# Optimization experiments

Hardware: AMD Instinct MI355X
Metric: run time of the kernel (lower is better)

## Reference

```python
import jax, jax.numpy as jnp
import numpy as np

B, T, D, H = 256, 512, 128, 256

def setup_inputs() -> dict:
    key = jax.random.key(0)
    ks = jax.random.split(key, 10)
    s_in = 1.0 / np.sqrt(H + D)
    s_td = 1.0 / np.sqrt(D)
    return {
        "x": jax.random.normal(ks[0], (B, T, D), dtype=jnp.float32),
        "delta": jax.random.uniform(ks[1], (B, T, D), dtype=jnp.float32),
        "W_mu": jax.random.uniform(ks[2], (H + D, H), minval=-s_in, maxval=s_in),
        "b_mu": jax.random.uniform(ks[3], (H,), minval=-s_in, maxval=s_in),
        "W_r": jax.random.uniform(ks[4], (H + D, H), minval=-s_in, maxval=s_in),
        "b_r": jax.random.uniform(ks[5], (H,), minval=-s_in, maxval=s_in),
        "W_h": jax.random.uniform(ks[6], (H + D, H), minval=-s_in, maxval=s_in),
        "b_h": jax.random.uniform(ks[7], (H,), minval=-s_in, maxval=s_in),
        "W_td": jax.random.uniform(ks[8], (D, H), minval=-s_td, maxval=s_td),
        "b_td": jax.random.uniform(ks[9], (H,), minval=-s_td, maxval=s_td),
    }

def reference(x, delta, W_mu, b_mu, W_r, b_r, W_h, b_h, W_td, b_td):
    # GRU-D style GRUI encoder; dropout is identity (eval mode).
    # Precompute temporal decay for all steps at once: beta [B,T,H]
    beta = jnp.exp(-jax.nn.relu(jnp.einsum('btd,dh->bth', delta, W_td) + b_td))
    # Precompute the x-part of the gate GEMMs (W split: first H rows act on h, last D on x)
    Wh_r, Wx_r = W_r[:H], W_r[H:]
    Wh_mu, Wx_mu = W_mu[:H], W_mu[H:]
    Wh_h, Wx_h = W_h[:H], W_h[H:]
    gx_r = jnp.einsum('btd,dh->bth', x, Wx_r) + b_r    # [B,T,H]
    gx_mu = jnp.einsum('btd,dh->bth', x, Wx_mu) + b_mu
    gx_h = jnp.einsum('btd,dh->bth', x, Wx_h) + b_h

    def step(h, inputs):
        beta_t, gxr_t, gxm_t, gxh_t = inputs
        h = beta_t * h
        r_t = jax.nn.sigmoid(h @ Wh_r + gxr_t)
        mu_t = jax.nn.sigmoid(h @ Wh_mu + gxm_t)
        h_hat = jnp.tanh((r_t * h) @ Wh_h + gxh_t)
        h = (1.0 - mu_t) * h + mu_t * h_hat
        return h, None

    h0 = jnp.zeros((x.shape[0], H), dtype=x.dtype)
    seq = (beta.transpose(1, 0, 2), gx_r.transpose(1, 0, 2),
           gx_mu.transpose(1, 0, 2), gx_h.transpose(1, 0, 2))
    h_T, _ = jax.lax.scan(step, h0, seq)
    return h_T
```

## Files before the change

kernel.cpp:

```cpp
#include <hip/hip_runtime.h>
#include <stdint.h>

#define TT 512
#define HB 256
#define DD 128

typedef _Float16 h2_t __attribute__((ext_vector_type(2)));
typedef _Float16 h8_t __attribute__((ext_vector_type(8)));
typedef float    f4_t __attribute__((ext_vector_type(4)));
typedef uint32_t u4_t __attribute__((ext_vector_type(4)));

#define GX_SZ 67108864ull


__device__ __forceinline__ uint32_t pack_h2f(float lo, float hi) {
  h2_t h; h[0] = (_Float16)lo; h[1] = (_Float16)hi;
  return __builtin_bit_cast(uint32_t, h);
}

__device__ __forceinline__ float fdot2f(uint32_t a, uint32_t b, float c) {
  h2_t ha = __builtin_bit_cast(h2_t, a), hb = __builtin_bit_cast(h2_t, b);
#if __has_builtin(__builtin_amdgcn_fdot2)
  return __builtin_amdgcn_fdot2(ha, hb, c, false);
#else
  return c + (float)ha[0]*(float)hb[0] + (float)ha[1]*(float)hb[1];
#endif
}

__device__ __forceinline__ void barrier_lds() {
  asm volatile("s_waitcnt lgkmcnt(0)" ::: "memory");
  __builtin_amdgcn_s_barrier();
  __builtin_amdgcn_sched_barrier(0);
}

__global__ __launch_bounds__(256)
void pack_w(const float* __restrict__ Wr, const float* __restrict__ Wmu,
            const float* __restrict__ Wh, const float* __restrict__ Wtd,
            uint8_t* __restrict__ bt) {
  const int id = blockIdx.x * 256 + threadIdx.x;
  const int a = id >> 14, rem = id & 16383;
  const int c = rem >> 6, kp = rem & 63;
  const float* W = (a==0) ? Wr : (a==1) ? Wmu : (a==2) ? Wh : Wtd;
  const int r0 = (a==3) ? 0 : 256;
  const uint32_t v = pack_h2f(W[(r0 + 2*kp)*256 + c], W[(r0 + 2*kp + 1)*256 + c]);
  *(uint32_t*)(bt + a*65536 + c*256 + ((kp*4) ^ ((c & 7) << 4))) = v;
}

__global__ __launch_bounds__(256, 2)
void gemm_pre(const float* __restrict__ x, const float* __restrict__ delta,
              const float* __restrict__ br, const float* __restrict__ bmu,
              const float* __restrict__ bh, const float* __restrict__ btd,
              const uint8_t* __restrict__ bt, uint8_t* __restrict__ ws) {
  __shared__ uint8_t BT[65536];
  const int a  = blockIdx.x & 3;
  const int m0 = (blockIdx.x >> 2) * 128;
  const int tid = threadIdx.x;
  const int l = tid & 63, w = tid >> 6;
  const float* Asrc = (a == 3) ? delta : x;
  const float* bias = (a==0) ? br : (a==1) ? bmu : (a==2) ? bh : btd;

  {
    const u4_t* s4 = (const u4_t*)(bt + (size_t)a*65536);
    u4_t* d4 = (u4_t*)BT;
    #pragma unroll
    for (int i = 0; i < 16; i++) d4[i*256 + tid] = s4[i*256 + tid];
  }
  __syncthreads();

  f4_t acc[2][16];
  #pragma unroll
  for (int rt = 0; rt < 2; rt++)
    #pragma unroll
    for (int nt = 0; nt < 16; nt++) acc[rt][nt] = (f4_t){0.f, 0.f, 0.f, 0.f};

  const int rbase = m0 + w*32 + (l & 15);
  #pragma unroll
  for (int ks = 0; ks < 4; ks++) {
    h8_t af[2];
    #pragma unroll
    for (int rt = 0; rt < 2; rt++) {
      const float* ap = Asrc + (size_t)(rbase + rt*16)*128 + ks*32 + (l >> 4)*8;
      f4_t f0 = *(const f4_t*)ap;
      f4_t f1 = *(const f4_t*)(ap + 4);
      h8_t v;
      v[0]=(_Float16)f0[0]; v[1]=(_Float16)f0[1]; v[2]=(_Float16)f0[2]; v[3]=(_Float16)f0[3];
      v[4]=(_Float16)f1[0]; v[5]=(_Float16)f1[1]; v[6]=(_Float16)f1[2]; v[7]=(_Float16)f1[3];
      af[rt] = v;
    }
    #pragma unroll
    for (int nt = 0; nt < 16; nt++) {
      const int c = nt*16 + (l & 15);
      const int boff = c*256 + ((ks*64 + (l >> 4)*16) ^ ((c & 7) << 4));
      h8_t bf = __builtin_bit_cast(h8_t, *(const u4_t*)(BT + boff));
      acc[0][nt] = __builtin_amdgcn_mfma_f32_16x16x32_f16(af[0], bf, acc[0][nt], 0, 0, 0);
      acc[1][nt] = __builtin_amdgcn_mfma_f32_16x16x32_f16(af[1], bf, acc[1][nt], 0, 0, 0);
    }
  }

  _Float16* outp = (_Float16*)(ws + (size_t)a * GX_SZ);
  #pragma unroll
  for (int nt = 0; nt < 16; nt++) {
    const int c = nt*16 + (l & 15);
    const float bv = bias[c];
    #pragma unroll
    for (int rt = 0; rt < 2; rt++) {
      #pragma unroll
      for (int i = 0; i < 4; i++) {
        const int row = m0 + w*32 + rt*16 + (l >> 4)*4 + i;
        float z = acc[rt][nt][i] + bv;
        if (a == 3) z = __expf(-fmaxf(z, 0.f));
        outp[(size_t)row*256 + c] = (_Float16)z;
      }
    }
  }
}

__global__ __launch_bounds__(512, 2)
void scan_k(const uint8_t* __restrict__ ws,
            const float* __restrict__ Wr, const float* __restrict__ Wmu,
            const float* __restrict__ Wh, float* __restrict__ out) {
  const int b = blockIdx.x;
  const int tid = threadIdx.x;
  const int l = tid & 63, w = tid >> 6, kq = l >> 3;

  __shared__ float hbf[256];
  __shared__ float muv[256];
  __shared__ u4_t  hb4[40];
  __shared__ u4_t  rh4[40];

  const int g   = w >> 2;
  const int cP1 = (w & 3)*64 + (l & 7) + 8*kq;
  const int cD  = w*32 + (l & 7) + 8*(kq & 3);

  const float* WG = (g == 0) ? Wr : Wmu;
  const int cb  = (w & 3)*64 + (l & 7);
  const int cb2 = w*32 + (l & 7);
  uint32_t w1[8][16];
  #pragma unroll
  for (int p = 0; p < 16; p++) {
    const int r = 2*(kq*16 + p);
    #pragma unroll
    for (int j = 0; j < 8; j++)
      w1[j][p] = pack_h2f(WG[r*256 + cb + 8*j], WG[(r+1)*256 + cb + 8*j]);
  }
  uint32_t w2[4][16];
  #pragma unroll
  for (int p = 0; p < 16; p++) {
    const int r = 2*(kq*16 + p);
    #pragma unroll
    for (int j = 0; j < 4; j++)
      w2[j][p] = pack_h2f(Wh[r*256 + cb2 + 8*j], Wh[(r+1)*256 + cb2 + 8*j]);
  }

  if (tid < 40)  hb4[tid] = (u4_t){0, 0, 0, 0};
  if (tid < 256) hbf[tid] = 0.f;

  const uint32_t rowbase = (uint32_t)b * (TT*HB) * 2u;
  const uint32_t gxP1off = (uint32_t)g * (uint32_t)GX_SZ + rowbase + (uint32_t)cP1*2u;
  const uint32_t gxhoff  = 2u*(uint32_t)GX_SZ + rowbase + (uint32_t)cD*2u;
  const uint32_t betoff  = 3u*(uint32_t)GX_SZ + rowbase + (uint32_t)(cD & ~1)*2u;
  const bool fin2 = (l < 32);
  const bool evn2 = fin2 && ((l & 1) == 0);

  uint16_t gxA  = *(const uint16_t*)(ws + gxP1off);
  uint16_t gxhA = fin2 ? *(const uint16_t*)(ws + gxhoff) : (uint16_t)0;
  uint32_t bA   = evn2 ? *(const uint32_t*)(ws + betoff + 1u*512u) : 0u;
  uint32_t bB   = evn2 ? *(const uint32_t*)(ws + betoff + 2u*512u) : 0u;

  __syncthreads();

  #pragma unroll 1
  for (int t = 0; t < TT; t++) {
    const int tn  = (t < TT-1) ? t+1 : TT-1;
    const int tn3 = (t < TT-3) ? t+3 : TT-1;
    uint16_t gxN  = *(const uint16_t*)(ws + gxP1off + (uint32_t)tn*512u);
    uint16_t gxhN = fin2 ? *(const uint16_t*)(ws + gxhoff + (uint32_t)tn*512u) : (uint16_t)0;
    uint32_t bC   = evn2 ? *(const uint32_t*)(ws + betoff + (uint32_t)tn3*512u) : 0u;

    float acc[8] = {0,0,0,0,0,0,0,0};
    #pragma unroll
    for (int q = 0; q < 4; q++) {
      u4_t hp = hb4[kq*5 + q];
      #pragma unroll
      for (int e = 0; e < 4; e++) {
        const uint32_t hv = hp[e];
        #pragma unroll
        for (int j = 0; j < 8; j++) acc[j] = fdot2f(w1[j][q*4 + e], hv, acc[j]);
      }
    }
    #pragma unroll
    for (int i = 0; i < 4; i++) {
      float snd = (l & 32) ? acc[i] : acc[i+4];
      float rcv = __shfl_xor(snd, 32, 64);
      acc[i] = ((l & 32) ? acc[i+4] : acc[i]) + rcv;
    }
    #pragma unroll
    for (int i = 0; i < 2; i++) {
      float snd = (l & 16) ? acc[i] : acc[i+2];
      float rcv = __shfl_xor(snd, 16, 64);
      acc[i] = ((l & 16) ? acc[i+2] : acc[i]) + rcv;
    }
    {
      float snd = (l & 8) ? acc[0] : acc[1];
      float rcv = __shfl_xor(snd, 8, 64);
      acc[0] = ((l & 8) ? acc[1] : acc[0]) + rcv;
    }
    {
      const float z = acc[0] + (float)__builtin_bit_cast(_Float16, gxA);
      const float v = 1.f / (1.f + __expf(-z));
      const float vn = __shfl_down(v, 1, 64);
      if (g == 1) {
        muv[cP1] = v;
      } else if ((l & 1) == 0) {
        const float rh0 = v  * hbf[cP1];
        const float rh1 = vn * hbf[cP1 + 1];
        const int pp = cP1 >> 1;
        ((uint32_t*)rh4)[(pp >> 4)*20 + (pp & 15)] = pack_h2f(rh0, rh1);
      }
    }
    barrier_lds();

    float a2[4] = {0,0,0,0};
    #pragma unroll
    for (int q = 0; q < 4; q++) {
      u4_t hp = rh4[kq*5 + q];
      #pragma unroll
      for (int e = 0; e < 4; e++) {
        const uint32_t hv = hp[e];
        #pragma unroll
        for (int j = 0; j < 4; j++) a2[j] = fdot2f(w2[j][q*4 + e], hv, a2[j]);
      }
    }
    #pragma unroll
    for (int i = 0; i < 4; i++) a2[i] += __shfl_xor(a2[i], 32, 64);
    #pragma unroll
    for (int i = 0; i < 2; i++) {
      float snd = (l & 16) ? a2[i] : a2[i+2];
      float rcv = __shfl_xor(snd, 16, 64);
      a2[i] = ((l & 16) ? a2[i+2] : a2[i]) + rcv;
    }
    {
      float snd = (l & 8) ? a2[0] : a2[1];
      float rcv = __shfl_xor(snd, 8, 64);
      a2[0] = ((l & 8) ? a2[1] : a2[0]) + rcv;
    }
    {
      const float z2 = a2[0] + (float)__builtin_bit_cast(_Float16, gxhA);
      const float e2 = __expf(2.f * z2);
      const float hh = 1.f - 2.f / (e2 + 1.f);
      const float hbv = hbf[cD];
      const float hn  = hbv + muv[cD] * (hh - hbv);
      const float hn1 = __shfl_down(hn, 1, 64);
      if (evn2) {
        const h2_t bp = __builtin_bit_cast(h2_t, bA);
        const float hb0 = (float)bp[0] * hn;
        const float hb1 = (float)bp[1] * hn1;
        const int pp = cD >> 1;
        ((uint32_t*)hb4)[(pp >> 4)*20 + (pp & 15)] = pack_h2f(hb0, hb1);
        hbf[cD]     = hb0;
        hbf[cD + 1] = hb1;
        if (t == TT-1) {
          out[b*256 + cD]     = hn;
          out[b*256 + cD + 1] = hn1;
        }
      }
    }
    gxA = gxN; gxhA = gxhN; bA = bB; bB = bC;
    barrier_lds();
  }
}

extern "C" void kernel_launch(void* const* d_in, const int* in_sizes, int n_in,
                              void* d_out, int out_size, void* d_ws, size_t ws_size,
                              hipStream_t stream) {
  const float* x    = (const float*)d_in[0];
  const float* delta= (const float*)d_in[1];
  const float* Wmu  = (const float*)d_in[2];
  const float* bmu  = (const float*)d_in[3];
  const float* Wr   = (const float*)d_in[4];
  const float* br   = (const float*)d_in[5];
  const float* Wh   = (const float*)d_in[6];
  const float* bh   = (const float*)d_in[7];
  const float* Wtd  = (const float*)d_in[8];
  const float* btd  = (const float*)d_in[9];
  uint8_t* ws = (uint8_t*)d_ws;
  uint8_t* bt = (uint8_t*)d_out;
  float* out = (float*)d_out;

  hipLaunchKernelGGL(pack_w,   dim3(256),  dim3(256), 0, stream, Wr, Wmu, Wh, Wtd, bt);
  hipLaunchKernelGGL(gemm_pre, dim3(4096), dim3(256), 0, stream, x, delta, br, bmu, bh, btd, bt, ws);
  hipLaunchKernelGGL(scan_k,   dim3(256),  dim3(512), 0, stream, ws, Wr, Wmu, Wh, out);
}
```

Before: 1.101 ms.

## Remap scan lanes so reductions use DPP and swizzle instead of wide shuffles

Reassigns lanes so the k-split index sits in the low three lane bits and output columns in the high bits. The cross-lane reductions of the recurrent GEMVs can then use DPP quad permutes and ds_swizzle rather than xor-shuffles over 32/16/8 lanes. The beta prefetch depth drops from three steps to two, and h is stored with float2 writes. This is meant to cut latency on the serial per-timestep critical path, but changes the weight-load pattern and makes more lanes do redundant loads and epilogue work.

```diff
diff --git a/kernel.cpp b/kernel.cpp
--- a/kernel.cpp
+++ b/kernel.cpp
@@ -12,19 +12,32 @@
 
 #define GX_SZ 67108864ull
 
-
 __device__ __forceinline__ uint32_t pack_h2f(float lo, float hi) {
   h2_t h; h[0] = (_Float16)lo; h[1] = (_Float16)hi;
   return __builtin_bit_cast(uint32_t, h);
 }
 
 __device__ __forceinline__ float fdot2f(uint32_t a, uint32_t b, float c) {
-  h2_t ha = __builtin_bit_cast(h2_t, a), hb = __builtin_bit_cast(h2_t, b);
 #if __has_builtin(__builtin_amdgcn_fdot2)
-  return __builtin_amdgcn_fdot2(ha, hb, c, false);
+  return __builtin_amdgcn_fdot2(__builtin_bit_cast(h2_t, a),
+                                __builtin_bit_cast(h2_t, b), c, false);
 #else
-  return c + (float)ha[0]*(float)hb[0] + (float)ha[1]*(float)hb[1];
+  asm("v_dot2_f32_f16 %0, %1, %2, %0" : "+v"(c) : "v"(a), "v"(b));
+  return c;
 #endif
+}
+
+__device__ __forceinline__ float dpp_xor1(float x) {
+  return __builtin_bit_cast(float, __builtin_amdgcn_update_dpp(
+      0, __builtin_bit_cast(int, x), 0xB1, 0xF, 0xF, true));
+}
+__device__ __forceinline__ float dpp_xor2(float x) {
+  return __builtin_bit_cast(float, __builtin_amdgcn_update_dpp(
+      0, __builtin_bit_cast(int, x), 0x4E, 0xF, 0xF, true));
+}
+__device__ __forceinline__ float swz_xor4(float x) {
+  return __builtin_bit_cast(float, __builtin_amdgcn_ds_swizzle(
+      __builtin_bit_cast(int, x), 0x101F));
 }
 
 __device__ __forceinline__ void barrier_lds() {
@@ -115,69 +128,71 @@
   }
 }
 
-__global__ __launch_bounds__(512, 2)
+__global__ __launch_bounds__(512)
+__attribute__((amdgpu_waves_per_eu(2, 2)))
 void scan_k(const uint8_t* __restrict__ ws,
             const float* __restrict__ Wr, const float* __restrict__ Wmu,
             const float* __restrict__ Wh, float* __restrict__ out) {
   const int b = blockIdx.x;
   const int tid = threadIdx.x;
-  const int l = tid & 63, w = tid >> 6, kq = l >> 3;
-
-  __shared__ float hbf[256];
+  const int l = tid & 63, w = tid >> 6;
+  const int kq = l & 7, co = l >> 3;
+  const int b0 = l & 1, b1 = (l >> 1) & 1, b2 = (l >> 2) & 1;
+
+  __shared__ __align__(16) float hbf[256];
   __shared__ float muv[256];
   __shared__ u4_t  hb4[40];
   __shared__ u4_t  rh4[40];
 
-  const int g   = w >> 2;
-  const int cP1 = (w & 3)*64 + (l & 7) + 8*kq;
-  const int cD  = w*32 + (l & 7) + 8*(kq & 3);
+  const int g = w >> 2;
+  const int c1 = (w & 3)*64 + l;
+  const int cD = w*32 + co*4 + (l & 3);
 
   const float* WG = (g == 0) ? Wr : Wmu;
-  const int cb  = (w & 3)*64 + (l & 7);
-  const int cb2 = w*32 + (l & 7);
-  uint32_t w1[8][16];
+  uint32_t w1b[8][16];
   #pragma unroll
   for (int p = 0; p < 16; p++) {
-    const int r = 2*(kq*16 + p);
-    #pragma unroll
-    for (int j = 0; j < 8; j++)
-      w1[j][p] = pack_h2f(WG[r*256 + cb + 8*j], WG[(r+1)*256 + cb + 8*j]);
-  }
-  uint32_t w2[4][16];
+    const int r0 = kq*32 + 2*p;
+    #pragma unroll
+    for (int j = 0; j < 8; j++) {
+      const int c = (w & 3)*64 + co*8 + j;
+      w1b[j][p] = pack_h2f(WG[r0*256 + c], WG[(r0+1)*256 + c]);
+    }
+  }
+  uint32_t w2b[4][16];
   #pragma unroll
   for (int p = 0; p < 16; p++) {
-    const int r = 2*(kq*16 + p);
-    #pragma unroll
-    for (int j = 0; j < 4; j++)
-      w2[j][p] = pack_h2f(Wh[r*256 + cb2 + 8*j], Wh[(r+1)*256 + cb2 + 8*j]);
+    const int r0 = kq*32 + 2*p;
+    #pragma unroll
+    for (int j = 0; j < 4; j++) {
+      const int c = w*32 + co*4 + j;
+      w2b[j][p] = pack_h2f(Wh[r0*256 + c], Wh[(r0+1)*256 + c]);
+    }
   }
 
   if (tid < 40)  hb4[tid] = (u4_t){0, 0, 0, 0};
   if (tid < 256) hbf[tid] = 0.f;
 
   const uint32_t rowbase = (uint32_t)b * (TT*HB) * 2u;
-  const uint32_t gxP1off = (uint32_t)g * (uint32_t)GX_SZ + rowbase + (uint32_t)cP1*2u;
+  const uint32_t gxP1off = (uint32_t)g * (uint32_t)GX_SZ + rowbase + (uint32_t)c1*2u;
   const uint32_t gxhoff  = 2u*(uint32_t)GX_SZ + rowbase + (uint32_t)cD*2u;
   const uint32_t betoff  = 3u*(uint32_t)GX_SZ + rowbase + (uint32_t)(cD & ~1)*2u;
-  const bool fin2 = (l < 32);
-  const bool evn2 = fin2 && ((l & 1) == 0);
 
   uint16_t gxA  = *(const uint16_t*)(ws + gxP1off);
-  uint16_t gxhA = fin2 ? *(const uint16_t*)(ws + gxhoff) : (uint16_t)0;
-  uint32_t bA   = evn2 ? *(const uint32_t*)(ws + betoff + 1u*512u) : 0u;
-  uint32_t bB   = evn2 ? *(const uint32_t*)(ws + betoff + 2u*512u) : 0u;
+  uint16_t gxhA = *(const uint16_t*)(ws + gxhoff);
+  uint32_t bA   = *(const uint32_t*)(ws + betoff + 1u*512u);
 
   __syncthreads();
 
   #pragma unroll 1
   for (int t = 0; t < TT; t++) {
     const int tn  = (t < TT-1) ? t+1 : TT-1;
-    const int tn3 = (t < TT-3) ? t+3 : TT-1;
+    const int tn2 = (t < TT-2) ? t+2 : TT-1;
     uint16_t gxN  = *(const uint16_t*)(ws + gxP1off + (uint32_t)tn*512u);
-    uint16_t gxhN = fin2 ? *(const uint16_t*)(ws + gxhoff + (uint32_t)tn*512u) : (uint16_t)0;
-    uint32_t bC   = evn2 ? *(const uint32_t*)(ws + betoff + (uint32_t)tn3*512u) : 0u;
-
-    float acc[8] = {0,0,0,0,0,0,0,0};
+    uint16_t gxhN = *(const uint16_t*)(ws + gxhoff + (uint32_t)tn*512u);
+    uint32_t bN   = *(const uint32_t*)(ws + betoff + (uint32_t)tn2*512u);
+
+    float a8[8] = {0,0,0,0,0,0,0,0};
     #pragma unroll
     for (int q = 0; q < 4; q++) {
       u4_t hp = hb4[kq*5 + q];
@@ -185,42 +200,46 @@
       for (int e = 0; e < 4; e++) {
         const uint32_t hv = hp[e];
         #pragma unroll
-        for (int j = 0; j < 8; j++) acc[j] = fdot2f(w1[j][q*4 + e], hv, acc[j]);
-      }
-    }
-    #pragma unroll
-    for (int i = 0; i < 4; i++) {
-      float snd = (l & 32) ? acc[i] : acc[i+4];
-      float rcv = __shfl_xor(snd, 32, 64);
-      acc[i] = ((l & 32) ? acc[i+4] : acc[i]) + rcv;
-    }
-    #pragma unroll
-    for (int i = 0; i < 2; i++) {
-      float snd = (l & 16) ? acc[i] : acc[i+2];
-      float rcv = __shfl_xor(snd, 16, 64);
-      acc[i] = ((l & 16) ? acc[i+2] : acc[i]) + rcv;
+        for (int j = 0; j < 8; j++) a8[j] = fdot2f(w1b[j][q*4 + e], hv, a8[j]);
+      }
+    }
+    float s4[4];
+    #pragma unroll
+    for (int j = 0; j < 4; j++) {
+      const float keep = b0 ? a8[2*j+1] : a8[2*j];
+      const float snd  = b0 ? a8[2*j]   : a8[2*j+1];
+      s4[j] = keep + dpp_xor1(snd);
+    }
+    float s2[2];
+    #pragma unroll
+    for (int j = 0; j < 2; j++) {
+      const float keep = b1 ? s4[2*j+1] : s4[2*j];
+      const float snd  = b1 ? s4[2*j]   : s4[2*j+1];
+      s2[j] = keep + dpp_xor2(snd);
     }
     {
-      float snd = (l & 8) ? acc[0] : acc[1];
-      float rcv = __shfl_xor(snd, 8, 64);
-      acc[0] = ((l & 8) ? acc[1] : acc[0]) + rcv;
-    }
-    {
-      const float z = acc[0] + (float)__builtin_bit_cast(_Float16, gxA);
+      const float keep = b2 ? s2[1] : s2[0];
+      const float snd  = b2 ? s2[0] : s2[1];
+      const float sum = keep + swz_xor4(snd);
+
+      const float z = sum + (float)__builtin_bit_cast(_Float16, gxA);
       const float v = 1.f / (1.f + __expf(-z));
-      const float vn = __shfl_down(v, 1, 64);
       if (g == 1) {
-        muv[cP1] = v;
-      } else if ((l & 1) == 0) {
-        const float rh0 = v  * hbf[cP1];
-        const float rh1 = vn * hbf[cP1 + 1];
-        const int pp = cP1 >> 1;
-        ((uint32_t*)rh4)[(pp >> 4)*20 + (pp & 15)] = pack_h2f(rh0, rh1);
+        muv[c1] = v;
+      } else {
+        const float vn = dpp_xor1(v);
+        const float2 hb2 = *(const float2*)&hbf[c1 & ~1];
+        const float rh0 = v  * hb2.x;
+        const float rh1 = vn * hb2.y;
+        if (b0 == 0) {
+          const int pp = c1 >> 1;
+          ((uint32_t*)rh4)[(pp >> 4)*20 + (pp & 15)] = pack_h2f(rh0, rh1);
+        }
       }
     }
     barrier_lds();
 
-    float a2[4] = {0,0,0,0};
+    float d4v[4] = {0,0,0,0};
     #pragma unroll
     for (int q = 0; q < 4; q++) {
       u4_t hp = rh4[kq*5 + q];
@@ -228,44 +247,42 @@
       for (int e = 0; e < 4; e++) {
         const uint32_t hv = hp[e];
         #pragma unroll
-        for (int j = 0; j < 4; j++) a2[j] = fdot2f(w2[j][q*4 + e], hv, a2[j]);
-      }
-    }
-    #pragma unroll
-    for (int i = 0; i < 4; i++) a2[i] += __shfl_xor(a2[i], 32, 64);
-    #pragma unroll
-    for (int i = 0; i < 2; i++) {
-      float snd = (l & 16) ? a2[i] : a2[i+2];
-      float rcv = __shfl_xor(snd, 16, 64);
-      a2[i] = ((l & 16) ? a2[i+2] : a2[i]) + rcv;
-    }
+        for (int j = 0; j < 4; j++) d4v[j] = fdot2f(w2b[j][q*4 + e], hv, d4v[j]);
+      }
+    }
+    float t2[2];
+    #pragma unroll
+    for (int j = 0; j < 2; j++) {
+      const float keep = b0 ? d4v[2*j+1] : d4v[2*j];
+      const float snd  = b0 ? d4v[2*j]   : d4v[2*j+1];
+      t2[j] = keep + dpp_xor1(snd);
+    }
+    float t1;
     {
-      float snd = (l & 8) ? a2[0] : a2[1];
-      float rcv = __shfl_xor(snd, 8, 64);
-      a2[0] = ((l & 8) ? a2[1] : a2[0]) + rcv;
-    }
+      const float keep = b1 ? t2[1] : t2[0];
+      const float snd  = b1 ? t2[0] : t2[1];
+      t1 = keep + dpp_xor2(snd);
+    }
+    const float sum2 = t1 + swz_xor4(t1);
+
     {
-      const float z2 = a2[0] + (float)__builtin_bit_cast(_Float16, gxhA);
+      const float z2 = sum2 + (float)__builtin_bit_cast(_Float16, gxhA);
       const float e2 = __expf(2.f * z2);
       const float hh = 1.f - 2.f / (e2 + 1.f);
       const float hbv = hbf[cD];
       const float hn  = hbv + muv[cD] * (hh - hbv);
-      const float hn1 = __shfl_down(hn, 1, 64);
-      if (evn2) {
+      const float vn  = dpp_xor1(hn);
+      if ((l & 5) == 0) {
         const h2_t bp = __builtin_bit_cast(h2_t, bA);
         const float hb0 = (float)bp[0] * hn;
-        const float hb1 = (float)bp[1] * hn1;
+        const float hb1 = (float)bp[1] * vn;
         const int pp = cD >> 1;
         ((uint32_t*)hb4)[(pp >> 4)*20 + (pp & 15)] = pack_h2f(hb0, hb1);
-        hbf[cD]     = hb0;
-        hbf[cD + 1] = hb1;
-        if (t == TT-1) {
-          out[b*256 + cD]     = hn;
-          out[b*256 + cD + 1] = hn1;
-        }
-      }
-    }
-    gxA = gxN; gxhA = gxhN; bA = bB; bB = bC;
+        *(float2*)&hbf[cD] = (float2){hb0, hb1};
+        if (t == TT-1) *(float2*)(out + b*256 + cD) = (float2){hn, vn};
+      }
+    }
+    gxA = gxN; gxhA = gxhN; bA = bN;
     barrier_lds();
   }
 }
```

After: 1.006 ms. 8.7% less time.
